# Kernel optimization log

Hardware: AMD Instinct MI355X
Metric: run time of the kernel (lower is better)

## Reference

```python
import jax, jax.numpy as jnp
import numpy as np
import math

D_MODEL = 1024
H = 16
D_H = D_MODEL // H
B, T = 1, 4096


def setup_inputs() -> dict:
    key = jax.random.key(0)
    ks = jax.random.split(key, 9)
    s = 1.0 / math.sqrt(D_MODEL)
    return {
        "x": jax.random.normal(ks[0], (B, T, D_MODEL), dtype=jnp.float32),
        "W_q": jax.random.normal(ks[1], (D_MODEL, D_MODEL), dtype=jnp.float32) * s,
        "b_q": jax.random.normal(ks[2], (D_MODEL,), dtype=jnp.float32) * 0.01,
        "W_k": jax.random.normal(ks[3], (D_MODEL, D_MODEL), dtype=jnp.float32) * s,
        "b_k": jax.random.normal(ks[4], (D_MODEL,), dtype=jnp.float32) * 0.01,
        "W_v": jax.random.normal(ks[5], (D_MODEL, D_MODEL), dtype=jnp.float32) * s,
        "b_v": jax.random.normal(ks[6], (D_MODEL,), dtype=jnp.float32) * 0.01,
        "W_o": jax.random.normal(ks[7], (D_MODEL, D_MODEL), dtype=jnp.float32) * s,
        "b_o": jax.random.normal(ks[8], (D_MODEL,), dtype=jnp.float32) * 0.01,
    }


def reference(x, W_q, b_q, W_k, b_k, W_v, b_v, W_o, b_o):
    b, t, _ = x.shape
    # torch nn.Linear: y = x @ W.T + b
    Q = x @ W_q.T + b_q  # (B, T, d_model)
    K = x @ W_k.T + b_k
    V = x @ W_v.T + b_v
    # split heads -> (B, h, T, d_h)
    Q = Q.reshape(b, t, H, D_H).transpose(0, 2, 1, 3)
    K = K.reshape(b, t, H, D_H).transpose(0, 2, 1, 3)
    V = V.reshape(b, t, H, D_H).transpose(0, 2, 1, 3)
    # scores (B, h, T, T)
    S = jnp.einsum("bhqd,bhkd->bhqk", Q, K) / math.sqrt(D_H)
    # causal mask: disallow k > q
    causal = jnp.tril(jnp.ones((t, t), dtype=bool))  # True = keep
    S = jnp.where(causal, S, -jnp.inf)
    A = jax.nn.softmax(S, axis=-1)
    Y = jnp.einsum("bhqk,bhkd->bhqd", A, V)  # (B, h, T, d_h)
    Y = Y.transpose(0, 2, 1, 3).reshape(b, t, D_MODEL)
    return Y @ W_o.T + b_o
```

## Files before the change

kernel.cpp:

```cpp
#include <hip/hip_runtime.h>


#define TSZ 4096
#define DM  1024
#define NH  16
#define DH  64
#define QSCALE 0.18033688f

typedef __bf16 bf16x8 __attribute__((ext_vector_type(8)));
typedef float  f32x4  __attribute__((ext_vector_type(4)));

__device__ __forceinline__ unsigned short f2bf(float x) {
    __bf16 h = (__bf16)x;
    return __builtin_bit_cast(unsigned short, h);
}

__device__ __forceinline__ uint4 pack8(const float4 a, const float4 b) {
    uint4 r;
    r.x = (unsigned)f2bf(a.x) | ((unsigned)f2bf(a.y) << 16);
    r.y = (unsigned)f2bf(a.z) | ((unsigned)f2bf(a.w) << 16);
    r.z = (unsigned)f2bf(b.x) | ((unsigned)f2bf(b.y) << 16);
    r.w = (unsigned)f2bf(b.z) | ((unsigned)f2bf(b.w) << 16);
    return r;
}

__device__ __forceinline__ int sw(int row, int cb) {
    return row * 64 + ((cb ^ ((row & 7) << 4)) >> 1);
}

__device__ __forceinline__ void gll16(const unsigned short* g, unsigned short* l) {
    __builtin_amdgcn_global_load_lds((const __attribute__((address_space(1))) void*)g,
                                     (__attribute__((address_space(3))) void*)l,
                                     16, 0, 0);
}

template <int CTRL>
__device__ __forceinline__ float dpp_f(float v) {
    return __builtin_bit_cast(float,
        __builtin_amdgcn_update_dpp(0, __builtin_bit_cast(int, v), CTRL, 0xF, 0xF, true));
}
__device__ __forceinline__ float red_sum16(float v) {
    v += dpp_f<0xB1>(v);
    v += dpp_f<0x4E>(v);
    v += dpp_f<0x124>(v);
    v += dpp_f<0x128>(v);
    return v;
}

#define XN  4194304u
#define WN  1048576u
__global__ __launch_bounds__(256)
void cvt_kernel(const float* __restrict__ x,  const float* __restrict__ wq,
                const float* __restrict__ wk, const float* __restrict__ wv,
                const float* __restrict__ wo,
                unsigned short* __restrict__ xb,  unsigned short* __restrict__ wqb,
                unsigned short* __restrict__ wkb, unsigned short* __restrict__ wvb,
                unsigned short* __restrict__ wob) {
    size_t e = ((size_t)blockIdx.x * 256 + threadIdx.x) * 8;
    const float* src; unsigned short* dst; size_t off;
    if (e < XN)               { src = x;  dst = xb;  off = e; }
    else if (e < XN + WN)     { src = wq; dst = wqb; off = e - XN; }
    else if (e < XN + 2 * WN) { src = wk; dst = wkb; off = e - XN - WN; }
    else if (e < XN + 3 * WN) { src = wv; dst = wvb; off = e - XN - 2 * WN; }
    else                      { src = wo; dst = wob; off = e - XN - 3 * WN; }
    float4 a = *reinterpret_cast<const float4*>(src + off);
    float4 b = *reinterpret_cast<const float4*>(src + off + 4);
    *reinterpret_cast<uint4*>(dst + off) = pack8(a, b);
}

__global__ __launch_bounds__(256)
void qkv_kernel(const unsigned short* __restrict__ xb,
                const unsigned short* __restrict__ wqb,
                const unsigned short* __restrict__ wkb,
                const unsigned short* __restrict__ wvb,
                const float* __restrict__ bq, const float* __restrict__ bk,
                const float* __restrict__ bv,
                unsigned short* __restrict__ qw,
                unsigned short* __restrict__ kw,
                unsigned short* __restrict__ vtw) {
    const int L = blockIdx.x;
    const int xcd = L & 7, i = L >> 3;
    const int lbx = i % 3, by = i / 3;
    const int bx = xcd * 3 + lbx;
    const int z = bx >> 3;
    const int col0 = (bx & 7) * 128;
    const int row0 = by * 128;

    const unsigned short* W = (z == 0) ? wqb : (z == 1) ? wkb : wvb;
    const float* bias = (z == 0) ? bq : (z == 1) ? bk : bv;
    unsigned short* outp = (z == 0) ? qw : (z == 1) ? kw : vtw;
    const float scale = (z == 0) ? QSCALE : 1.0f;

    __shared__ unsigned short Al[128 * 64];
    __shared__ unsigned short Bl[128 * 64];

    const int tid = threadIdx.x;
    const int wid = tid >> 6, lane = tid & 63, g = lane >> 4, l15 = lane & 15;
    const int wr = (wid >> 1) * 64, wc = (wid & 1) * 64;

    f32x4 acc[4][4];
#pragma unroll
    for (int m = 0; m < 4; ++m)
#pragma unroll
        for (int n = 0; n < 4; ++n) acc[m][n] = (f32x4){0.f, 0.f, 0.f, 0.f};

    const int r_ = tid >> 3, c8_ = tid & 7;
    const int cbyte = (c8_ * 16) ^ ((r_ & 7) << 4);
    const unsigned short* ga0 = xb + (size_t)(row0 + r_) * DM + (cbyte >> 1);
    const unsigned short* gb0 = W + (size_t)(col0 + r_) * DM + (cbyte >> 1);
    unsigned short* la0 = &Al[(size_t)(wid * 64) * 8];
    unsigned short* lb0 = &Bl[(size_t)(wid * 64) * 8];

    for (int kt = 0; kt < DM; kt += 64) {
#pragma unroll
        for (int is = 0; is < 4; ++is) {
            gll16(ga0 + (size_t)(is * 32) * DM + kt, la0 + (size_t)(is * 256) * 8);
            gll16(gb0 + (size_t)(is * 32) * DM + kt, lb0 + (size_t)(is * 256) * 8);
        }
        __syncthreads();
#pragma unroll
        for (int kk = 0; kk < 2; ++kk) {
            bf16x8 a[4], b[4];
#pragma unroll
            for (int m = 0; m < 4; ++m)
                a[m] = *reinterpret_cast<const bf16x8*>(&Al[sw(wr + m * 16 + l15, kk * 64 + 16 * g)]);
#pragma unroll
            for (int n = 0; n < 4; ++n)
                b[n] = *reinterpret_cast<const bf16x8*>(&Bl[sw(wc + n * 16 + l15, kk * 64 + 16 * g)]);
            if (z == 2) {
#pragma unroll
                for (int m = 0; m < 4; ++m)
#pragma unroll
                    for (int n = 0; n < 4; ++n)
                        acc[m][n] = __builtin_amdgcn_mfma_f32_16x16x32_bf16(b[n], a[m], acc[m][n], 0, 0, 0);
            } else {
#pragma unroll
                for (int m = 0; m < 4; ++m)
#pragma unroll
                    for (int n = 0; n < 4; ++n)
                        acc[m][n] = __builtin_amdgcn_mfma_f32_16x16x32_bf16(a[m], b[n], acc[m][n], 0, 0, 0);
            }
        }
        __syncthreads();
    }

    if (z == 2) {
#pragma unroll
        for (int n = 0; n < 4; ++n)
#pragma unroll
            for (int r = 0; r < 4; ++r) {
                int ch = col0 + wc + n * 16 + 4 * g + r;
                float bval = bias[ch];
#pragma unroll
                for (int m = 0; m < 4; ++m) {
                    int t = row0 + wr + m * 16 + l15;
                    outp[(size_t)ch * TSZ + t] = f2bf(acc[m][n][r] + bval);
                }
            }
    } else {
#pragma unroll
        for (int n = 0; n < 4; ++n) {
            int col = col0 + wc + n * 16 + l15;
            float bval = bias[col];
            int hh = col >> 6, dd = col & 63;
#pragma unroll
            for (int m = 0; m < 4; ++m) {
                int rbase = row0 + wr + m * 16 + 4 * g;
#pragma unroll
                for (int r = 0; r < 4; ++r)
                    outp[((size_t)hh * TSZ + rbase + r) * DH + dd] = f2bf((acc[m][n][r] + bval) * scale);
            }
        }
    }
}

__global__ __launch_bounds__(256, 4)
void attn_kernel(const unsigned short* __restrict__ qw,
                 const unsigned short* __restrict__ kw,
                 const unsigned short* __restrict__ vtw,
                 unsigned short* __restrict__ yw) {
    __shared__ unsigned short Qs[64 * 64];
    __shared__ unsigned short Ks[2][64 * 64];
    __shared__ unsigned short Vs[2][64 * 64];

    const int L = blockIdx.x;
    const int xcd = L & 7, k = L >> 3;
    const int h = xcd + 8 * (k & 1);
    const int qt = 63 - (k >> 1);
    const int tid = threadIdx.x;
    const int wid = tid >> 6, lane = tid & 63, g = lane >> 4, l15 = lane & 15;

    const unsigned short* qbase = qw + (size_t)h * TSZ * DH;
    const unsigned short* kbase = kw + (size_t)h * TSZ * DH;
    const unsigned short* vbase = vtw + (size_t)h * DH * TSZ;

    const int r0 = tid >> 3;
    const int cc = (tid & 7) ^ (r0 & 7);
    const int klo = r0 * 64 + cc * 8;
    const size_t vlo = (size_t)r0 * TSZ + cc * 8;

    {
        const unsigned short* qsrc = qbase + (size_t)qt * 64 * DH;
#pragma unroll
        for (int i2 = 0; i2 < 2; ++i2) {
            int c = tid + i2 * 256;
            int r = c >> 3, c8 = c & 7;
            *reinterpret_cast<uint4*>(&Qs[sw(r, c8 * 16)]) =
                *reinterpret_cast<const uint4*>(qsrc + c * 8);
            *reinterpret_cast<uint4*>(&Ks[0][sw(r, c8 * 16)]) =
                *reinterpret_cast<const uint4*>(kbase + c * 8);
            *reinterpret_cast<uint4*>(&Vs[0][sw(r, c8 * 16)]) =
                *reinterpret_cast<const uint4*>(vbase + (size_t)r * TSZ + c8 * 8);
        }
    }
    __syncthreads();

    bf16x8 aq[2];
    aq[0] = *reinterpret_cast<const bf16x8*>(&Qs[sw(wid * 16 + l15, 16 * g)]);
    aq[1] = *reinterpret_cast<const bf16x8*>(&Qs[sw(wid * 16 + l15, 64 + 16 * g)]);
    __syncthreads();

    float l_st[4];
    f32x4 accO[4];
#pragma unroll
    for (int r = 0; r < 4; ++r) l_st[r] = 0.f;
#pragma unroll
    for (int n = 0; n < 4; ++n) accO[n] = (f32x4){0.f, 0.f, 0.f, 0.f};

    for (int j = 0; j <= qt; ++j) {
        const int cur = j & 1;
        if (j < qt) {
            const unsigned short* ks = kbase + (size_t)(j + 1) * 64 * DH + klo;
            const unsigned short* vs = vbase + (size_t)(j + 1) * 64 + vlo;
            unsigned short* kb = &Ks[cur ^ 1][wid * 512];
            unsigned short* vb = &Vs[cur ^ 1][wid * 512];
            gll16(ks, kb);
            gll16(ks + 2048, kb + 2048);
            gll16(vs, vb);
            gll16(vs + (size_t)32 * TSZ, vb + 2048);
        }

        f32x4 sacc[4];
#pragma unroll
        for (int n = 0; n < 4; ++n) sacc[n] = (f32x4){0.f, 0.f, 0.f, 0.f};
        __builtin_amdgcn_s_setprio(1);
#pragma unroll
        for (int kk = 0; kk < 2; ++kk) {
#pragma unroll
            for (int n = 0; n < 4; ++n) {
                bf16x8 bk = *reinterpret_cast<const bf16x8*>(&Ks[cur][sw(n * 16 + l15, kk * 64 + 16 * g)]);
                sacc[n] = __builtin_amdgcn_mfma_f32_16x16x32_bf16(aq[kk], bk, sacc[n], 0, 0, 0);
            }
        }
        __builtin_amdgcn_s_setprio(0);
        if (j == qt) {
#pragma unroll
            for (int n = 0; n < 4; ++n)
#pragma unroll
                for (int r = 0; r < 4; ++r)
                    if (n * 16 + l15 > wid * 16 + 4 * g + r) sacc[n][r] = -__builtin_inff();
        }

        float p[4][4];
#pragma unroll
        for (int r = 0; r < 4; ++r) {
            float rs = 0.f;
#pragma unroll
            for (int n = 0; n < 4; ++n) { p[n][r] = exp2f(sacc[n][r]); rs += p[n][r]; }
            l_st[r] += rs;
        }

#pragma unroll
        for (int n = 0; n < 4; ++n)
#pragma unroll
            for (int r = 0; r < 4; ++r)
                Qs[sw(wid * 16 + 4 * g + r, (n * 16 + l15) * 2)] = f2bf(p[n][r]);

        __builtin_amdgcn_s_setprio(1);
#pragma unroll
        for (int kk = 0; kk < 2; ++kk) {
            bf16x8 pa = *reinterpret_cast<const bf16x8*>(&Qs[sw(wid * 16 + l15, kk * 64 + 16 * g)]);
#pragma unroll
            for (int n = 0; n < 4; ++n) {
                bf16x8 bv = *reinterpret_cast<const bf16x8*>(&Vs[cur][sw(n * 16 + l15, kk * 64 + 16 * g)]);
                accO[n] = __builtin_amdgcn_mfma_f32_16x16x32_bf16(pa, bv, accO[n], 0, 0, 0);
            }
        }
        __builtin_amdgcn_s_setprio(0);
        __syncthreads();
    }

#pragma unroll
    for (int r = 0; r < 4; ++r) {
        float lt = red_sum16(l_st[r]);
        float inv = 1.0f / lt;
        int row = qt * 64 + wid * 16 + 4 * g + r;
#pragma unroll
        for (int n = 0; n < 4; ++n)
            yw[(size_t)row * DM + h * DH + n * 16 + l15] = f2bf(accO[n][r] * inv);
    }
}

__global__ __launch_bounds__(256)
void oproj_kernel(const unsigned short* __restrict__ y,
                  const unsigned short* __restrict__ wob,
                  const float* __restrict__ bo,
                  float* __restrict__ out) {
    const int L = blockIdx.x;
    const int xcd = L & 7, i = L >> 3;
    const int bx = i & 7, lby = i >> 3;
    const int by = xcd * 4 + lby;
    const int row0 = by * 128, col0 = bx * 128;

    __shared__ unsigned short Al[128 * 64];
    __shared__ unsigned short Bl[128 * 64];

    const int tid = threadIdx.x;
    const int wid = tid >> 6, lane = tid & 63, g = lane >> 4, l15 = lane & 15;
    const int wr = (wid >> 1) * 64, wc = (wid & 1) * 64;

    f32x4 acc[4][4];
#pragma unroll
    for (int m = 0; m < 4; ++m)
#pragma unroll
        for (int n = 0; n < 4; ++n) acc[m][n] = (f32x4){0.f, 0.f, 0.f, 0.f};

    const int r_ = tid >> 3, c8_ = tid & 7;
    const int cbyte = (c8_ * 16) ^ ((r_ & 7) << 4);
    const unsigned short* ga0 = y + (size_t)(row0 + r_) * DM + (cbyte >> 1);
    const unsigned short* gb0 = wob + (size_t)(col0 + r_) * DM + (cbyte >> 1);
    unsigned short* la0 = &Al[(size_t)(wid * 64) * 8];
    unsigned short* lb0 = &Bl[(size_t)(wid * 64) * 8];

    for (int kt = 0; kt < DM; kt += 64) {
#pragma unroll
        for (int is = 0; is < 4; ++is) {
            gll16(ga0 + (size_t)(is * 32) * DM + kt, la0 + (size_t)(is * 256) * 8);
            gll16(gb0 + (size_t)(is * 32) * DM + kt, lb0 + (size_t)(is * 256) * 8);
        }
        __syncthreads();
#pragma unroll
        for (int kk = 0; kk < 2; ++kk) {
            bf16x8 a[4], b[4];
#pragma unroll
            for (int m = 0; m < 4; ++m)
                a[m] = *reinterpret_cast<const bf16x8*>(&Al[sw(wr + m * 16 + l15, kk * 64 + 16 * g)]);
#pragma unroll
            for (int n = 0; n < 4; ++n)
                b[n] = *reinterpret_cast<const bf16x8*>(&Bl[sw(wc + n * 16 + l15, kk * 64 + 16 * g)]);
#pragma unroll
            for (int m = 0; m < 4; ++m)
#pragma unroll
                for (int n = 0; n < 4; ++n)
                    acc[m][n] = __builtin_amdgcn_mfma_f32_16x16x32_bf16(a[m], b[n], acc[m][n], 0, 0, 0);
        }
        __syncthreads();
    }

#pragma unroll
    for (int n = 0; n < 4; ++n) {
        int col = col0 + wc + n * 16 + l15;
        float bval = bo[col];
#pragma unroll
        for (int m = 0; m < 4; ++m) {
            int rbase = row0 + wr + m * 16 + 4 * g;
#pragma unroll
            for (int r = 0; r < 4; ++r)
                out[(size_t)(rbase + r) * DM + col] = acc[m][n][r] + bval;
        }
    }
}

extern "C" void kernel_launch(void* const* d_in, const int* in_sizes, int n_in,
                              void* d_out, int out_size, void* d_ws, size_t ws_size,
                              hipStream_t stream) {
    const float* x  = (const float*)d_in[0];
    const float* Wq = (const float*)d_in[1];
    const float* bq = (const float*)d_in[2];
    const float* Wk = (const float*)d_in[3];
    const float* bk = (const float*)d_in[4];
    const float* Wv = (const float*)d_in[5];
    const float* bv = (const float*)d_in[6];
    const float* Wo = (const float*)d_in[7];
    const float* bo = (const float*)d_in[8];
    float* out = (float*)d_out;

    unsigned short* xb  = (unsigned short*)d_ws;
    unsigned short* wqb = xb + 4194304;
    unsigned short* wkb = wqb + 1048576;
    unsigned short* wvb = wkb + 1048576;
    unsigned short* wob = wvb + 1048576;
    unsigned short* qw  = wob + 1048576;
    unsigned short* kw  = qw + 4194304;
    unsigned short* vtw = kw + 4194304;
    unsigned short* yw  = xb;

    cvt_kernel<<<4096, 256, 0, stream>>>(x, Wq, Wk, Wv, Wo, xb, wqb, wkb, wvb, wob);
    qkv_kernel<<<768, 256, 0, stream>>>(xb, wqb, wkb, wvb, bq, bk, bv, qw, kw, vtw);
    attn_kernel<<<1024, 256, 0, stream>>>(qw, kw, vtw, yw);
    oproj_kernel<<<256, 256, 0, stream>>>(yw, wob, bo, out);
}
```

Before: 148.4 us.

## Split attention key dimension across waves, keep P in registers, reduce via LDS atomics

Restructures the attention kernel so each wave owns a 16-key slice of every K/V tile and computes S transposed (K as the A operand), which lets the P fragment feed the 16x16x16 MFMA for PV straight from registers. This removes the per-iteration LDS write and read-back of P. Each wave now keeps partial O and row sums for all 64 query rows, and these are combined at the end through float atomicAdds into LDS before normalizing. The cost is four times as many accumulator registers, with occupancy lowered from 4 to 3 blocks per CU, plus a final LDS atomic reduction.

```diff
diff --git a/kernel.cpp b/kernel.cpp
--- a/kernel.cpp
+++ b/kernel.cpp
@@ -8,6 +8,7 @@
 #define QSCALE 0.18033688f
 
 typedef __bf16 bf16x8 __attribute__((ext_vector_type(8)));
+typedef __bf16 bf16x4 __attribute__((ext_vector_type(4)));
 typedef float  f32x4  __attribute__((ext_vector_type(4)));
 
 __device__ __forceinline__ unsigned short f2bf(float x) {
@@ -34,17 +35,11 @@
                                      16, 0, 0);
 }
 
-template <int CTRL>
-__device__ __forceinline__ float dpp_f(float v) {
-    return __builtin_bit_cast(float,
-        __builtin_amdgcn_update_dpp(0, __builtin_bit_cast(int, v), CTRL, 0xF, 0xF, true));
-}
-__device__ __forceinline__ float red_sum16(float v) {
-    v += dpp_f<0xB1>(v);
-    v += dpp_f<0x4E>(v);
-    v += dpp_f<0x124>(v);
-    v += dpp_f<0x128>(v);
-    return v;
+__device__ __forceinline__ f32x4 mfma16(bf16x4 a, bf16x4 b, f32x4 c) {
+    f32x4 d;
+    asm("v_mfma_f32_16x16x16_bf16 %0, %1, %2, %3"
+        : "=v"(d) : "v"(a), "v"(b), "0"(c));
+    return d;
 }
 
 #define XN  4194304u
@@ -174,7 +169,7 @@
     }
 }
 
-__global__ __launch_bounds__(256, 4)
+__global__ __launch_bounds__(256, 3)
 void attn_kernel(const unsigned short* __restrict__ qw,
                  const unsigned short* __restrict__ kw,
                  const unsigned short* __restrict__ vtw,
@@ -215,17 +210,19 @@
     }
     __syncthreads();
 
-    bf16x8 aq[2];
-    aq[0] = *reinterpret_cast<const bf16x8*>(&Qs[sw(wid * 16 + l15, 16 * g)]);
-    aq[1] = *reinterpret_cast<const bf16x8*>(&Qs[sw(wid * 16 + l15, 64 + 16 * g)]);
-    __syncthreads();
-
-    float l_st[4];
-    f32x4 accO[4];
-#pragma unroll
-    for (int r = 0; r < 4; ++r) l_st[r] = 0.f;
-#pragma unroll
-    for (int n = 0; n < 4; ++n) accO[n] = (f32x4){0.f, 0.f, 0.f, 0.f};
+    bf16x8 aq[4][2];
+#pragma unroll
+    for (int qb = 0; qb < 4; ++qb)
+#pragma unroll
+        for (int kk = 0; kk < 2; ++kk)
+            aq[qb][kk] = *reinterpret_cast<const bf16x8*>(&Qs[sw(qb * 16 + l15, kk * 64 + 16 * g)]);
+
+    float l_st[4] = {0.f, 0.f, 0.f, 0.f};
+    f32x4 accO[4][4];
+#pragma unroll
+    for (int qb = 0; qb < 4; ++qb)
+#pragma unroll
+        for (int nd = 0; nd < 4; ++nd) accO[qb][nd] = (f32x4){0.f, 0.f, 0.f, 0.f};
 
     for (int j = 0; j <= qt; ++j) {
         const int cur = j & 1;
@@ -242,62 +239,79 @@
 
         f32x4 sacc[4];
 #pragma unroll
-        for (int n = 0; n < 4; ++n) sacc[n] = (f32x4){0.f, 0.f, 0.f, 0.f};
+        for (int qb = 0; qb < 4; ++qb) sacc[qb] = (f32x4){0.f, 0.f, 0.f, 0.f};
         __builtin_amdgcn_s_setprio(1);
 #pragma unroll
         for (int kk = 0; kk < 2; ++kk) {
-#pragma unroll
-            for (int n = 0; n < 4; ++n) {
-                bf16x8 bk = *reinterpret_cast<const bf16x8*>(&Ks[cur][sw(n * 16 + l15, kk * 64 + 16 * g)]);
-                sacc[n] = __builtin_amdgcn_mfma_f32_16x16x32_bf16(aq[kk], bk, sacc[n], 0, 0, 0);
-            }
+            bf16x8 bk = *reinterpret_cast<const bf16x8*>(&Ks[cur][sw(16 * wid + l15, kk * 64 + 16 * g)]);
+#pragma unroll
+            for (int qb = 0; qb < 4; ++qb)
+                sacc[qb] = __builtin_amdgcn_mfma_f32_16x16x32_bf16(bk, aq[qb][kk], sacc[qb], 0, 0, 0);
         }
         __builtin_amdgcn_s_setprio(0);
         if (j == qt) {
 #pragma unroll
-            for (int n = 0; n < 4; ++n)
+            for (int qb = 0; qb < 4; ++qb)
 #pragma unroll
                 for (int r = 0; r < 4; ++r)
-                    if (n * 16 + l15 > wid * 16 + 4 * g + r) sacc[n][r] = -__builtin_inff();
-        }
-
-        float p[4][4];
-#pragma unroll
-        for (int r = 0; r < 4; ++r) {
-            float rs = 0.f;
-#pragma unroll
-            for (int n = 0; n < 4; ++n) { p[n][r] = exp2f(sacc[n][r]); rs += p[n][r]; }
-            l_st[r] += rs;
-        }
-
-#pragma unroll
-        for (int n = 0; n < 4; ++n)
-#pragma unroll
-            for (int r = 0; r < 4; ++r)
-                Qs[sw(wid * 16 + 4 * g + r, (n * 16 + l15) * 2)] = f2bf(p[n][r]);
+                    if (16 * wid + 4 * g + r > qb * 16 + l15) sacc[qb][r] = -__builtin_inff();
+        }
+
+        bf16x4 pfrag[4];
+#pragma unroll
+        for (int qb = 0; qb < 4; ++qb) {
+            float p0 = exp2f(sacc[qb][0]);
+            float p1 = exp2f(sacc[qb][1]);
+            float p2 = exp2f(sacc[qb][2]);
+            float p3 = exp2f(sacc[qb][3]);
+            l_st[qb] += (p0 + p1) + (p2 + p3);
+            unsigned w0, w1;
+            asm("v_cvt_pk_bf16_f32 %0, %1, %2" : "=v"(w0) : "v"(p0), "v"(p1));
+            asm("v_cvt_pk_bf16_f32 %0, %1, %2" : "=v"(w1) : "v"(p2), "v"(p3));
+            uint2 pw = make_uint2(w0, w1);
+            pfrag[qb] = __builtin_bit_cast(bf16x4, pw);
+        }
 
         __builtin_amdgcn_s_setprio(1);
 #pragma unroll
-        for (int kk = 0; kk < 2; ++kk) {
-            bf16x8 pa = *reinterpret_cast<const bf16x8*>(&Qs[sw(wid * 16 + l15, kk * 64 + 16 * g)]);
-#pragma unroll
-            for (int n = 0; n < 4; ++n) {
-                bf16x8 bv = *reinterpret_cast<const bf16x8*>(&Vs[cur][sw(n * 16 + l15, kk * 64 + 16 * g)]);
-                accO[n] = __builtin_amdgcn_mfma_f32_16x16x32_bf16(pa, bv, accO[n], 0, 0, 0);
-            }
+        for (int nd = 0; nd < 4; ++nd) {
+            bf16x4 bv = *reinterpret_cast<const bf16x4*>(&Vs[cur][sw(nd * 16 + l15, 32 * wid + 8 * g)]);
+#pragma unroll
+            for (int qb = 0; qb < 4; ++qb)
+                accO[qb][nd] = mfma16(pfrag[qb], bv, accO[qb][nd]);
         }
         __builtin_amdgcn_s_setprio(0);
         __syncthreads();
     }
 
-#pragma unroll
-    for (int r = 0; r < 4; ++r) {
-        float lt = red_sum16(l_st[r]);
-        float inv = 1.0f / lt;
-        int row = qt * 64 + wid * 16 + 4 * g + r;
-#pragma unroll
-        for (int n = 0; n < 4; ++n)
-            yw[(size_t)row * DM + h * DH + n * 16 + l15] = f2bf(accO[n][r] * inv);
+    float* Obuf = reinterpret_cast<float*>(&Ks[0][0]);
+    float* Lbuf = reinterpret_cast<float*>(&Vs[0][0]);
+    for (int i2 = tid; i2 < 64 * 64; i2 += 256) Obuf[i2] = 0.f;
+    if (tid < 64) Lbuf[tid] = 0.f;
+    __syncthreads();
+
+#pragma unroll
+    for (int qb = 0; qb < 4; ++qb) {
+        float lv = l_st[qb];
+        lv += __shfl_xor(lv, 16);
+        lv += __shfl_xor(lv, 32);
+        if (lane < 16) atomicAdd(&Lbuf[qb * 16 + lane], lv);
+    }
+#pragma unroll
+    for (int qb = 0; qb < 4; ++qb)
+#pragma unroll
+        for (int nd = 0; nd < 4; ++nd)
+#pragma unroll
+            for (int r = 0; r < 4; ++r)
+                atomicAdd(&Obuf[(qb * 16 + 4 * g + r) * 64 + nd * 16 + l15], accO[qb][nd][r]);
+    __syncthreads();
+
+#pragma unroll
+    for (int i2 = 0; i2 < 16; ++i2) {
+        int idx = i2 * 256 + tid;
+        int q = idx >> 6, d = idx & 63;
+        float inv = 1.0f / Lbuf[q];
+        yw[(size_t)(qt * 64 + q) * DM + h * DH + d] = f2bf(Obuf[q * 64 + d] * inv);
     }
 }
 
```

Result: slower. 209.2 us (+40.9%).
